# Performance work log

Measured on AMD Instinct MI355X. Metric: run time of the kernel, lower is better.

## Reference

```python
import jax, jax.numpy as jnp
import numpy as np

N_HEAD = 16

def setup_inputs() -> dict:
    key = jax.random.key(0)
    k1, k2, k3 = jax.random.split(key, 3)
    B, S, D = 2, 2048, 1024
    std = 0.02
    return {
        "hidden_states": jax.random.normal(k1, (B, S, D), jnp.float32),
        "w_attn": jax.random.normal(k2, (D, 3 * D), jnp.float32) * std,
        "b_attn": jnp.zeros((3 * D,), jnp.float32),
        "w_proj": jax.random.normal(k3, (D, D), jnp.float32) * std,
        "b_proj": jnp.zeros((D,), jnp.float32),
    }

def reference(hidden_states, w_attn, b_attn, w_proj, b_proj):
    B, S, D = hidden_states.shape
    H = N_HEAD
    hd = D // H
    # fused qkv projection (Conv1D == x @ W + b)
    qkv = hidden_states @ w_attn + b_attn            # [B,S,3D]
    q, k, v = jnp.split(qkv, 3, axis=-1)
    def split_heads(t):
        return t.reshape(B, S, H, hd).transpose(0, 2, 1, 3)  # [B,H,S,hd]
    q, k, v = split_heads(q), split_heads(k), split_heads(v)
    # scores with scale = sqrt(head_dim)
    scores = jnp.einsum('bhqd,bhkd->bhqk', q, k) / jnp.sqrt(jnp.asarray(hd, q.dtype))
    causal = jnp.tril(jnp.ones((S, S), bool))
    mask_value = jnp.finfo(scores.dtype).min
    scores = jnp.where(causal, scores, mask_value)
    attn = jax.nn.softmax(scores, axis=-1)           # dropout p=0 (eval)
    out = jnp.einsum('bhqk,bhkd->bhqd', attn, v)     # [B,H,S,hd]
    out = out.transpose(0, 2, 1, 3).reshape(B, S, D)
    out = out @ w_proj + b_proj
    return out
```

## Files before the change

### kernel.cpp

```cpp
#include <hip/hip_runtime.h>

#define S_LEN 2048
#define D_MODEL 1024
#define NHEAD 16
#define HDIM 64
#define BATCH 2
#define M_ROWS (BATCH * S_LEN)
#define N_QKV (3 * D_MODEL)
#define QSCALE 0.18033688011112042f

typedef __attribute__((ext_vector_type(8))) short bf16x8;
typedef __attribute__((ext_vector_type(4))) float f32x4;

static __device__ __forceinline__ unsigned short f2bf(float f) {
  unsigned int u = __float_as_uint(f);
  u += 0x7FFFu + ((u >> 16) & 1u);
  return (unsigned short)(u >> 16);
}
static __device__ __forceinline__ unsigned int pkbf(float a, float b) {
  unsigned int ua = __float_as_uint(a) + 0x8000u;
  unsigned int ub = __float_as_uint(b) + 0x8000u;
  return __builtin_amdgcn_perm(ub, ua, 0x07060302u);
}

static __device__ __forceinline__ void async_cp16(unsigned short* lds, const unsigned short* g) {
  __builtin_amdgcn_global_load_lds((__attribute__((address_space(1))) void*)g,
                                   (__attribute__((address_space(3))) void*)lds, 16, 0, 0);
}

__global__ __launch_bounds__(256) void k_prep(const float* __restrict__ x,
                                              unsigned short* __restrict__ xb,
                                              const float* __restrict__ w_attn,
                                              unsigned short* __restrict__ wqkvT,
                                              const float* __restrict__ w_proj,
                                              unsigned short* __restrict__ wprojT) {
  __shared__ unsigned short T[32][33];
  const int blk = blockIdx.x;
  const int tid = threadIdx.x;
  if (blk < 4096) {
    int i = blk * 256 + tid;
    float4 v = ((const float4*)x)[i];
    ushort4 o;
    o.x = f2bf(v.x); o.y = f2bf(v.y); o.z = f2bf(v.z); o.w = f2bf(v.w);
    ((ushort4*)xb)[i] = o;
    return;
  }
  const float* w;
  unsigned short* wT;
  int bid, Ndim;
  if (blk < 7168) { bid = blk - 4096; w = w_attn; wT = wqkvT; Ndim = N_QKV; }
  else            { bid = blk - 7168; w = w_proj; wT = wprojT; Ndim = D_MODEL; }
  const int nb = Ndim / 32;
  const int n0 = (bid % nb) * 32, k0 = (bid / nb) * 32;
  const int tx = tid & 31, ty = tid >> 5;
#pragma unroll
  for (int j = 0; j < 4; ++j) {
    int r = ty + j * 8;
    T[r][tx] = f2bf(w[(size_t)(k0 + r) * Ndim + n0 + tx]);
  }
  __syncthreads();
#pragma unroll
  for (int j = 0; j < 4; ++j) {
    int r = ty + j * 8;
    wT[(size_t)(n0 + r) * D_MODEL + k0 + tx] = T[tx][r];
  }
}

__global__ __launch_bounds__(256) void k_gemm_qkv(const unsigned short* __restrict__ A,
                                                  const unsigned short* __restrict__ Bt,
                                                  const float* __restrict__ bias,
                                                  unsigned short* __restrict__ Qb,
                                                  unsigned short* __restrict__ Kbuf,
                                                  unsigned short* __restrict__ VTb) {
  __shared__ __align__(16) unsigned short As[128 * 32];
  __shared__ __align__(16) unsigned short Bs[128 * 32];
  const int tid = threadIdx.x;
  const int wid = tid >> 6, lane = tid & 63;
  const int lr = lane & 15, lg = lane >> 4;
  const int bm = blockIdx.y * 128, bn = blockIdx.x * 128;
  const int wm = (wid >> 1) * 64, wn = (wid & 1) * 64;
  const int K = D_MODEL;
  const int c0 = tid, c1 = tid + 256;
  const size_t a0o = (size_t)(bm + (c0 >> 2)) * K + (c0 & 3) * 8;
  const size_t a1o = (size_t)(bm + (c1 >> 2)) * K + (c1 & 3) * 8;
  const size_t b0o = (size_t)(bn + (c0 >> 2)) * K + (c0 & 3) * 8;
  const size_t b1o = (size_t)(bn + (c1 >> 2)) * K + (c1 & 3) * 8;

  f32x4 acc[4][4] = {};

  for (int k0 = 0; k0 < K; k0 += 32) {
    __syncthreads();
    async_cp16(&As[c0 * 8], &A[a0o + k0]);
    async_cp16(&As[c1 * 8], &A[a1o + k0]);
    async_cp16(&Bs[c0 * 8], &Bt[b0o + k0]);
    async_cp16(&Bs[c1 * 8], &Bt[b1o + k0]);
    __syncthreads();
    bf16x8 af[4], bfr[4];
#pragma unroll
    for (int i = 0; i < 4; ++i) af[i] = *(const bf16x8*)&As[(wm + i * 16 + lr) * 32 + lg * 8];
#pragma unroll
    for (int t = 0; t < 4; ++t) bfr[t] = *(const bf16x8*)&Bs[(wn + t * 16 + lr) * 32 + lg * 8];
#pragma unroll
    for (int i = 0; i < 4; ++i)
#pragma unroll
      for (int t = 0; t < 4; ++t)
        acc[i][t] = __builtin_amdgcn_mfma_f32_16x16x32_bf16(af[i], bfr[t], acc[i][t], 0, 0, 0);
  }
#pragma unroll
  for (int i = 0; i < 4; ++i) {
#pragma unroll
    for (int t = 0; t < 4; ++t) {
      int n = bn + wn + t * 16 + lr;
      int part = n >> 10, rem = n & 1023;
      int h = rem >> 6, d = rem & 63;
      float bv = bias[n];
      int row0 = bm + wm + i * 16 + lg * 4;
      int bb = row0 >> 11, s0 = row0 & 2047;
      if (part == 2) {
        ushort4 vv;
        vv.x = f2bf(acc[i][t][0] + bv);
        vv.y = f2bf(acc[i][t][1] + bv);
        vv.z = f2bf(acc[i][t][2] + bv);
        vv.w = f2bf(acc[i][t][3] + bv);
        *(ushort4*)&VTb[(((size_t)(bb << 4) + h) * HDIM + d) * S_LEN + s0] = vv;
      } else {
        unsigned short* dst = (part == 0) ? Qb : Kbuf;
        float sc = (part == 0) ? QSCALE : 1.0f;
#pragma unroll
        for (int r = 0; r < 4; ++r)
          dst[(((size_t)(bb << 4) + h) * S_LEN + (s0 + r)) * HDIM + d] = f2bf((acc[i][t][r] + bv) * sc);
      }
    }
  }
}

__global__ __launch_bounds__(256) void k_gemm_proj(const unsigned short* __restrict__ A,
                                                   const unsigned short* __restrict__ Bt,
                                                   const float* __restrict__ bias,
                                                   float* __restrict__ out) {
  __shared__ __align__(16) unsigned short As[128 * 32];
  __shared__ __align__(16) unsigned short Bs[128 * 32];
  const int tid = threadIdx.x;
  const int wid = tid >> 6, lane = tid & 63;
  const int lr = lane & 15, lg = lane >> 4;
  const int bm = blockIdx.y * 128, bn = blockIdx.x * 128;
  const int wm = (wid >> 1) * 64, wn = (wid & 1) * 64;
  const int K = D_MODEL;
  const int c0 = tid, c1 = tid + 256;
  const size_t a0o = (size_t)(bm + (c0 >> 2)) * K + (c0 & 3) * 8;
  const size_t a1o = (size_t)(bm + (c1 >> 2)) * K + (c1 & 3) * 8;
  const size_t b0o = (size_t)(bn + (c0 >> 2)) * K + (c0 & 3) * 8;
  const size_t b1o = (size_t)(bn + (c1 >> 2)) * K + (c1 & 3) * 8;

  f32x4 acc[4][4] = {};

  for (int k0 = 0; k0 < K; k0 += 32) {
    __syncthreads();
    async_cp16(&As[c0 * 8], &A[a0o + k0]);
    async_cp16(&As[c1 * 8], &A[a1o + k0]);
    async_cp16(&Bs[c0 * 8], &Bt[b0o + k0]);
    async_cp16(&Bs[c1 * 8], &Bt[b1o + k0]);
    __syncthreads();
    bf16x8 af[4], bfr[4];
#pragma unroll
    for (int i = 0; i < 4; ++i) af[i] = *(const bf16x8*)&As[(wm + i * 16 + lr) * 32 + lg * 8];
#pragma unroll
    for (int t = 0; t < 4; ++t) bfr[t] = *(const bf16x8*)&Bs[(wn + t * 16 + lr) * 32 + lg * 8];
#pragma unroll
    for (int i = 0; i < 4; ++i)
#pragma unroll
      for (int t = 0; t < 4; ++t)
        acc[i][t] = __builtin_amdgcn_mfma_f32_16x16x32_bf16(af[i], bfr[t], acc[i][t], 0, 0, 0);
  }
#pragma unroll
  for (int i = 0; i < 4; ++i) {
#pragma unroll
    for (int t = 0; t < 4; ++t) {
      int n = bn + wn + t * 16 + lr;
      float bv = bias[n];
#pragma unroll
      for (int r = 0; r < 4; ++r) {
        int row = bm + wm + i * 16 + lg * 4 + r;
        out[(size_t)row * D_MODEL + n] = acc[i][t][r] + bv;
      }
    }
  }
}

__global__ __launch_bounds__(256, 2) void k_attn6(const unsigned short* __restrict__ Qb,
                                                  const unsigned short* __restrict__ Kb,
                                                  const unsigned short* __restrict__ VT,
                                                  unsigned short* __restrict__ AO) {
  const int tid = threadIdx.x;
  const int wid = tid >> 6, lane = tid & 63;
  const int lr = lane & 15, quad = lane >> 4;
  const int bh = blockIdx.x;
  const int slot = blockIdx.y;
  const int b = bh >> 4, h = bh & 15;

  __shared__ __align__(16) unsigned short Ks[64 * 64];
  __shared__ __align__(16) unsigned short Vs[64 * 64];
  __shared__ __align__(16) unsigned short Pbuf[4][16 * 72];
  unsigned short* pb = &Pbuf[wid][0];

  const unsigned short* Kbh = Kb + (size_t)bh * S_LEN * HDIM;
  const unsigned short* VTbh = VT + (size_t)bh * HDIM * S_LEN;

  const int sL = slot * 4 + wid;
  const int Rs[2] = {sL * 16, (127 - sL) * 16};
  const int ntile = ((127 - slot * 4) >> 2) + 1;

  bf16x8 qf[2][2];
#pragma unroll
  for (int st = 0; st < 2; ++st)
#pragma unroll
    for (int dh = 0; dh < 2; ++dh)
      qf[st][dh] = *(const bf16x8*)&Qb[((size_t)bh * S_LEN + Rs[st] + lr) * HDIM + dh * 32 + quad * 8];

  f32x4 Ot[2][4] = {};
  float ms[2] = {-1e30f, -1e30f};
  float ls[2] = {0.f, 0.f};

  const int srow = lane >> 3;
  const int scol = ((lane & 7) ^ srow) * 8;

  for (int kt = 0; kt < ntile; ++kt) {
    const int k0 = kt * 64;
    __syncthreads();
#pragma unroll
    for (int j = 0; j < 2; ++j) {
      const int r0 = wid * 16 + j * 8;
      async_cp16(&Ks[r0 * 64 + lane * 8], &Kbh[(size_t)(k0 + r0 + srow) * HDIM + scol]);
      async_cp16(&Vs[r0 * 64 + lane * 8], &VTbh[(size_t)(r0 + srow) * S_LEN + k0 + scol]);
    }
    __syncthreads();

    bf16x8 kf[4][2], vf[4][2];
#pragma unroll
    for (int kg = 0; kg < 4; ++kg)
#pragma unroll
      for (int dh = 0; dh < 2; ++dh)
        kf[kg][dh] = *(const bf16x8*)&Ks[(kg * 16 + lr) * 64 + (((dh * 4 + quad) ^ (lr & 7)) * 8)];
#pragma unroll
    for (int dg = 0; dg < 4; ++dg)
#pragma unroll
      for (int kh = 0; kh < 2; ++kh)
        vf[dg][kh] = *(const bf16x8*)&Vs[(dg * 16 + lr) * 64 + (((kh * 4 + quad) ^ (lr & 7)) * 8)];

#pragma unroll
    for (int st = 0; st < 2; ++st) {
      const int R = Rs[st];
      if (k0 > R + 15) continue;
      f32x4 Sv[4];
#pragma unroll
      for (int kg = 0; kg < 4; ++kg) {
        f32x4 a = {};
        a = __builtin_amdgcn_mfma_f32_16x16x32_bf16(kf[kg][0], qf[st][0], a, 0, 0, 0);
        a = __builtin_amdgcn_mfma_f32_16x16x32_bf16(kf[kg][1], qf[st][1], a, 0, 0, 0);
        Sv[kg] = a;
      }
      if (k0 + 63 > R) {
        const int q = R + lr;
#pragma unroll
        for (int kg = 0; kg < 4; ++kg)
#pragma unroll
          for (int r = 0; r < 4; ++r)
            if (k0 + kg * 16 + quad * 4 + r > q) Sv[kg][r] = -1e30f;
      }
      float mx = ms[st];
#pragma unroll
      for (int kg = 0; kg < 4; ++kg)
        mx = fmaxf(mx, fmaxf(fmaxf(Sv[kg][0], Sv[kg][1]), fmaxf(Sv[kg][2], Sv[kg][3])));
      mx = fmaxf(mx, __shfl_xor(mx, 16));
      mx = fmaxf(mx, __shfl_xor(mx, 32));
      const float alpha = __builtin_amdgcn_exp2f(ms[st] - mx);
      ms[st] = mx;
      float rs = 0.f;
#pragma unroll
      for (int kg = 0; kg < 4; ++kg) {
        float e0 = __builtin_amdgcn_exp2f(Sv[kg][0] - mx);
        float e1 = __builtin_amdgcn_exp2f(Sv[kg][1] - mx);
        float e2 = __builtin_amdgcn_exp2f(Sv[kg][2] - mx);
        float e3 = __builtin_amdgcn_exp2f(Sv[kg][3] - mx);
        rs += (e0 + e1) + (e2 + e3);
        *(unsigned int*)&pb[lr * 72 + kg * 16 + quad * 4]     = pkbf(e0, e1);
        *(unsigned int*)&pb[lr * 72 + kg * 16 + quad * 4 + 2] = pkbf(e2, e3);
      }
      rs += __shfl_xor(rs, 16);
      rs += __shfl_xor(rs, 32);
      ls[st] = ls[st] * alpha + rs;
#pragma unroll
      for (int dg = 0; dg < 4; ++dg)
#pragma unroll
        for (int r = 0; r < 4; ++r) Ot[st][dg][r] *= alpha;
      bf16x8 pf0 = *(const bf16x8*)&pb[lr * 72 + quad * 8];
      bf16x8 pf1 = *(const bf16x8*)&pb[lr * 72 + 32 + quad * 8];
#pragma unroll
      for (int dg = 0; dg < 4; ++dg) {
        Ot[st][dg] = __builtin_amdgcn_mfma_f32_16x16x32_bf16(vf[dg][0], pf0, Ot[st][dg], 0, 0, 0);
        Ot[st][dg] = __builtin_amdgcn_mfma_f32_16x16x32_bf16(vf[dg][1], pf1, Ot[st][dg], 0, 0, 0);
      }
    }
  }

#pragma unroll
  for (int st = 0; st < 2; ++st) {
    const float rl = __builtin_amdgcn_rcpf(ls[st]);
    const int s = Rs[st] + lr;
#pragma unroll
    for (int dg = 0; dg < 4; ++dg) {
      const size_t o = ((size_t)b * S_LEN + s) * D_MODEL + h * 64 + dg * 16 + quad * 4;
      *(unsigned int*)&AO[o]     = pkbf(Ot[st][dg][0] * rl, Ot[st][dg][1] * rl);
      *(unsigned int*)&AO[o + 2] = pkbf(Ot[st][dg][2] * rl, Ot[st][dg][3] * rl);
    }
  }
}

extern "C" void kernel_launch(void* const* d_in, const int* in_sizes, int n_in,
                              void* d_out, int out_size, void* d_ws, size_t ws_size,
                              hipStream_t stream) {
  const float* x      = (const float*)d_in[0];
  const float* w_attn = (const float*)d_in[1];
  const float* b_attn = (const float*)d_in[2];
  const float* w_proj = (const float*)d_in[3];
  const float* b_proj = (const float*)d_in[4];
  float* out = (float*)d_out;

  unsigned short* ws     = (unsigned short*)d_ws;
  unsigned short* xb     = ws;
  unsigned short* wqkvT  = xb + (size_t)M_ROWS * D_MODEL;
  unsigned short* wprojT = wqkvT + (size_t)N_QKV * D_MODEL;
  unsigned short* Qb     = wprojT + (size_t)D_MODEL * D_MODEL;
  unsigned short* Kb     = Qb + (size_t)M_ROWS * D_MODEL;
  unsigned short* VT     = Kb + (size_t)M_ROWS * D_MODEL;
  unsigned short* AO     = xb;

  k_prep<<<8192, 256, 0, stream>>>(x, xb, w_attn, wqkvT, w_proj, wprojT);
  k_gemm_qkv<<<dim3(N_QKV / 128, M_ROWS / 128), 256, 0, stream>>>(xb, wqkvT, b_attn, Qb, Kb, VT);
  k_attn6<<<dim3(BATCH * NHEAD, 16), 256, 0, stream>>>(Qb, Kb, VT, AO);
  k_gemm_proj<<<dim3(D_MODEL / 128, M_ROWS / 128), 256, 0, stream>>>(AO, wprojT, b_proj, out);
}
```

Baseline: 199.4 us.

## Double-buffer LDS tiles and remap GEMM blocks per XCD

Both projection GEMMs now use two LDS buffers per operand, prefetching the next K-slice while computing on the current one, and drop one barrier per iteration. Launch grids are flattened to 1D and block indices are remapped so each XCD works on a contiguous group of tiles, improving L2 reuse of A/B. This costs double the LDS per block and relies on the single barrier plus the copy's completion semantics for correctness.

Measured after the change: 179.9 us. 1.11x faster.

```diff
diff --git a/kernel.cpp b/kernel.cpp
--- a/kernel.cpp
+++ b/kernel.cpp
@@ -72,12 +72,15 @@
                                                   unsigned short* __restrict__ Qb,
                                                   unsigned short* __restrict__ Kbuf,
                                                   unsigned short* __restrict__ VTb) {
-  __shared__ __align__(16) unsigned short As[128 * 32];
-  __shared__ __align__(16) unsigned short Bs[128 * 32];
+  __shared__ __align__(16) unsigned short As[2][128 * 32];
+  __shared__ __align__(16) unsigned short Bs[2][128 * 32];
   const int tid = threadIdx.x;
   const int wid = tid >> 6, lane = tid & 63;
   const int lr = lane & 15, lg = lane >> 4;
-  const int bm = blockIdx.y * 128, bn = blockIdx.x * 128;
+  const int blk = blockIdx.x;
+  const int xcd = blk & 7, idx = blk >> 3;
+  const int bm = ((xcd & 3) * 8 + (idx & 7)) * 128;
+  const int bn = ((xcd >> 2) * 12 + (idx >> 3)) * 128;
   const int wm = (wid >> 1) * 64, wn = (wid & 1) * 64;
   const int K = D_MODEL;
   const int c0 = tid, c1 = tid + 256;
@@ -88,18 +91,25 @@
 
   f32x4 acc[4][4] = {};
 
+  async_cp16(&As[0][c0 * 8], &A[a0o]);
+  async_cp16(&As[0][c1 * 8], &A[a1o]);
+  async_cp16(&Bs[0][c0 * 8], &Bt[b0o]);
+  async_cp16(&Bs[0][c1 * 8], &Bt[b1o]);
+
   for (int k0 = 0; k0 < K; k0 += 32) {
+    const int p = (k0 >> 5) & 1;
     __syncthreads();
-    async_cp16(&As[c0 * 8], &A[a0o + k0]);
-    async_cp16(&As[c1 * 8], &A[a1o + k0]);
-    async_cp16(&Bs[c0 * 8], &Bt[b0o + k0]);
-    async_cp16(&Bs[c1 * 8], &Bt[b1o + k0]);
-    __syncthreads();
+    if (k0 + 32 < K) {
+      async_cp16(&As[p ^ 1][c0 * 8], &A[a0o + k0 + 32]);
+      async_cp16(&As[p ^ 1][c1 * 8], &A[a1o + k0 + 32]);
+      async_cp16(&Bs[p ^ 1][c0 * 8], &Bt[b0o + k0 + 32]);
+      async_cp16(&Bs[p ^ 1][c1 * 8], &Bt[b1o + k0 + 32]);
+    }
     bf16x8 af[4], bfr[4];
 #pragma unroll
-    for (int i = 0; i < 4; ++i) af[i] = *(const bf16x8*)&As[(wm + i * 16 + lr) * 32 + lg * 8];
-#pragma unroll
-    for (int t = 0; t < 4; ++t) bfr[t] = *(const bf16x8*)&Bs[(wn + t * 16 + lr) * 32 + lg * 8];
+    for (int i = 0; i < 4; ++i) af[i] = *(const bf16x8*)&As[p][(wm + i * 16 + lr) * 32 + lg * 8];
+#pragma unroll
+    for (int t = 0; t < 4; ++t) bfr[t] = *(const bf16x8*)&Bs[p][(wn + t * 16 + lr) * 32 + lg * 8];
 #pragma unroll
     for (int i = 0; i < 4; ++i)
 #pragma unroll
@@ -138,12 +148,15 @@
                                                    const unsigned short* __restrict__ Bt,
                                                    const float* __restrict__ bias,
                                                    float* __restrict__ out) {
-  __shared__ __align__(16) unsigned short As[128 * 32];
-  __shared__ __align__(16) unsigned short Bs[128 * 32];
+  __shared__ __align__(16) unsigned short As[2][128 * 32];
+  __shared__ __align__(16) unsigned short Bs[2][128 * 32];
   const int tid = threadIdx.x;
   const int wid = tid >> 6, lane = tid & 63;
   const int lr = lane & 15, lg = lane >> 4;
-  const int bm = blockIdx.y * 128, bn = blockIdx.x * 128;
+  const int blk = blockIdx.x;
+  const int xcd = blk & 7, idx = blk >> 3;
+  const int bm = (xcd * 4 + (idx & 3)) * 128;
+  const int bn = (idx >> 2) * 128;
   const int wm = (wid >> 1) * 64, wn = (wid & 1) * 64;
   const int K = D_MODEL;
   const int c0 = tid, c1 = tid + 256;
@@ -154,18 +167,25 @@
 
   f32x4 acc[4][4] = {};
 
+  async_cp16(&As[0][c0 * 8], &A[a0o]);
+  async_cp16(&As[0][c1 * 8], &A[a1o]);
+  async_cp16(&Bs[0][c0 * 8], &Bt[b0o]);
+  async_cp16(&Bs[0][c1 * 8], &Bt[b1o]);
+
   for (int k0 = 0; k0 < K; k0 += 32) {
+    const int p = (k0 >> 5) & 1;
     __syncthreads();
-    async_cp16(&As[c0 * 8], &A[a0o + k0]);
-    async_cp16(&As[c1 * 8], &A[a1o + k0]);
-    async_cp16(&Bs[c0 * 8], &Bt[b0o + k0]);
-    async_cp16(&Bs[c1 * 8], &Bt[b1o + k0]);
-    __syncthreads();
+    if (k0 + 32 < K) {
+      async_cp16(&As[p ^ 1][c0 * 8], &A[a0o + k0 + 32]);
+      async_cp16(&As[p ^ 1][c1 * 8], &A[a1o + k0 + 32]);
+      async_cp16(&Bs[p ^ 1][c0 * 8], &Bt[b0o + k0 + 32]);
+      async_cp16(&Bs[p ^ 1][c1 * 8], &Bt[b1o + k0 + 32]);
+    }
     bf16x8 af[4], bfr[4];
 #pragma unroll
-    for (int i = 0; i < 4; ++i) af[i] = *(const bf16x8*)&As[(wm + i * 16 + lr) * 32 + lg * 8];
-#pragma unroll
-    for (int t = 0; t < 4; ++t) bfr[t] = *(const bf16x8*)&Bs[(wn + t * 16 + lr) * 32 + lg * 8];
+    for (int i = 0; i < 4; ++i) af[i] = *(const bf16x8*)&As[p][(wm + i * 16 + lr) * 32 + lg * 8];
+#pragma unroll
+    for (int t = 0; t < 4; ++t) bfr[t] = *(const bf16x8*)&Bs[p][(wn + t * 16 + lr) * 32 + lg * 8];
 #pragma unroll
     for (int i = 0; i < 4; ++i)
 #pragma unroll
@@ -336,7 +356,7 @@
   unsigned short* AO     = xb;
 
   k_prep<<<8192, 256, 0, stream>>>(x, xb, w_attn, wqkvT, w_proj, wprojT);
-  k_gemm_qkv<<<dim3(N_QKV / 128, M_ROWS / 128), 256, 0, stream>>>(xb, wqkvT, b_attn, Qb, Kb, VT);
+  k_gemm_qkv<<<768, 256, 0, stream>>>(xb, wqkvT, b_attn, Qb, Kb, VT);
   k_attn6<<<dim3(BATCH * NHEAD, 16), 256, 0, stream>>>(Qb, Kb, VT, AO);
-  k_gemm_proj<<<dim3(D_MODEL / 128, M_ROWS / 128), 256, 0, stream>>>(AO, wprojT, b_proj, out);
-}
+  k_gemm_proj<<<256, 256, 0, stream>>>(AO, wprojT, b_proj, out);
+}
```
